# Performance work log

Measured on AMD Instinct MI355X. Metric: run time of the kernel, lower is better.

The kernel has to match this reference:

```python
import jax, jax.numpy as jnp
import numpy as np

TWOPI = 2.0 * np.pi


def setup_inputs() -> dict:
    key = jax.random.key(0)
    B, N, C = 16, 2048, 256
    x = jax.random.normal(key, (B, N, C), dtype=jnp.float32)
    return {"x": x}


def reference(x) -> jnp.ndarray:
    # Real-cosine DFT along dim 1: out[b,k,c] = sum_n x[b,n,c] * cos(-2*pi*n*k/N)
    # Equivalent to the original broadcast+sum but expressed as a GEMM with the
    # precomputed (N, N) cosine matrix (avoids the B*N*N*C intermediate).
    N = x.shape[1]
    n = jnp.arange(N, dtype=x.dtype)
    term = -TWOPI * n[None, :] * n[:, None] / N  # (k, n)
    cos_mat = jnp.cos(term)
    return jnp.einsum('kn,bnc->bkc', cos_mat, x)
```

## Files before the change

### kernel.cpp

```cpp
#include <hip/hip_runtime.h>
#include <hip/hip_bf16.h>
#include <math.h>

typedef __bf16 bf16_t;
typedef __attribute__((ext_vector_type(8))) __bf16 bf16x8;
typedef __attribute__((ext_vector_type(4))) float f32x4;

#define NN 2048
#define CC 256
#define BB 16
#define COLS 4096

#define KEE 320
#define MEE 256
#define KEO 256
#define KO  512

#define ANG2 (6.283185307179586f / 2048.0f)
#define ANG1 (6.283185307179586f / 1024.0f)
#define ANG0 (6.283185307179586f / 512.0f)

__device__ __forceinline__ void gload_lds16(const void* g, void* l) {
    __builtin_amdgcn_global_load_lds(
        (const __attribute__((address_space(1))) void*)g,
        (__attribute__((address_space(3))) void*)l, 16, 0, 0);
}

union V8 { bf16_t h[8]; uint4 v; };

#define NBLK_AEE 40
#define NBLK_AEO 32
#define NBLK_AO  128
#define NBLK_A   (NBLK_AEE + NBLK_AEO + NBLK_AO)
#define NBLK_FOLD 512
#define PREP_BLOCKS (NBLK_A + NBLK_FOLD + 64)

__global__ __launch_bounds__(256) void prep_kernel(
    const float* __restrict__ x,
    bf16_t* __restrict__ Aee, bf16_t* __restrict__ Aeo, bf16_t* __restrict__ Ao,
    bf16_t* __restrict__ Yee, bf16_t* __restrict__ Yeo, bf16_t* __restrict__ Yo)
{
    const int blk = blockIdx.x;
    const int t = threadIdx.x;

    if (blk < NBLK_AEE) {
        const int u = blk * 256 + t;
        const int i = u / 40;
        const int p0 = (u - i * 40) * 8;
        const unsigned step = (unsigned)i & 511u;
        unsigned ph = ((unsigned)i * (unsigned)p0) & 511u;
        V8 vals;
#pragma unroll
        for (int q = 0; q < 8; ++q) {
            vals.h[q] = (p0 + q <= 256) ? (bf16_t)cosf((float)ph * ANG0) : (bf16_t)0.0f;
            ph = (ph + step) & 511u;
        }
        *reinterpret_cast<uint4*>(Aee + (size_t)i * KEE + p0) = vals.v;
        return;
    }
    if (blk < NBLK_AEE + NBLK_AEO) {
        const int u = (blk - NBLK_AEE) * 256 + t;
        const int i = u >> 5;
        const int m0 = (u & 31) * 8;
        const unsigned tw = 2u * (unsigned)i + 1u;
        unsigned ph = ((unsigned)m0 * tw) & 1023u;
        V8 vals;
#pragma unroll
        for (int q = 0; q < 8; ++q) {
            vals.h[q] = (bf16_t)cosf((float)ph * ANG1);
            ph = (ph + tw) & 1023u;
        }
        *reinterpret_cast<uint4*>(Aeo + (size_t)i * KEO + m0) = vals.v;
        return;
    }
    if (blk < NBLK_A) {
        const int u = (blk - NBLK_AEE - NBLK_AEO) * 256 + t;
        const int j = u >> 6;
        const int u0 = (u & 63) * 8;
        const unsigned tw = 2u * (unsigned)j + 1u;
        V8 vals;
#pragma unroll
        for (int q = 0; q < 8; ++q) {
            const int uu = u0 + q;
            const int m = (uu <= 256) ? uu : (768 - uu);
            const unsigned ph = ((unsigned)m * tw) & 2047u;
            vals.h[q] = (bf16_t)cosf((float)ph * ANG2);
        }
        *reinterpret_cast<uint4*>(Ao + (size_t)j * KO + u0) = vals.v;
        return;
    }

    if (blk < NBLK_A + NBLK_FOLD) {
        const int f = blk - NBLK_A;
        const int pt = f >> 6;
        const int ct = f & 63;
        const int gc0 = ct * 64;
        const int col = t & 63;
        const int pg = t >> 6;
        const int p_base = pt * 32 + pg * 8;
        const float* xcol = x + (size_t)(gc0 >> 8) * NN * CC + (gc0 & 255) + col;

        float eeV[8], eoV[8], olV[8], ohV[8];
#pragma unroll
        for (int q = 0; q < 8; ++q) {
            const int p = p_base + q;
            const int n2 = 512 - p, n3 = 512 + p, n4 = 1024 - p;
            const int n5 = 1024 + p, n6 = 1536 - p, n7 = 1536 + p;
            const int n8 = (2048 - p) & 2047;
            const float x1 = xcol[(size_t)p  * CC];
            const float x2 = xcol[(size_t)n2 * CC];
            const float x3 = xcol[(size_t)n3 * CC];
            const float x4 = xcol[(size_t)n4 * CC];
            const float x5 = xcol[(size_t)n5 * CC];
            const float x6 = xcol[(size_t)n6 * CC];
            const float x7 = xcol[(size_t)n7 * CC];
            const float x8 = xcol[(size_t)n8 * CC];
            const float w = (p == 0) ? 0.5f : 1.0f;
            const float e_lo = w * ((x1 + x4) + (x5 + x8));
            const float e_hi = w * ((x2 + x3) + (x6 + x7));
            olV[q] = w * ((x1 - x5) - (x4 - x8));
            ohV[q] = (x2 - x6) - (x3 - x7);
            eeV[q] = e_lo + e_hi;
            eoV[q] = e_lo - e_hi;
        }
        if (pt == 0 && pg == 0) {
            const float a = xcol[(size_t)256  * CC];
            const float b2 = xcol[(size_t)768  * CC];
            const float c = xcol[(size_t)1280 * CC];
            const float d = xcol[(size_t)1792 * CC];
            ohV[0] = (a - c) - (b2 - d);
        }
        V8 vee, veo, vol, voh;
#pragma unroll
        for (int q = 0; q < 8; ++q) {
            vee.h[q] = (bf16_t)eeV[q]; veo.h[q] = (bf16_t)eoV[q];
            vol.h[q] = (bf16_t)olV[q]; voh.h[q] = (bf16_t)ohV[q];
        }
        const size_t gcol = (size_t)(gc0 + col);
        *reinterpret_cast<uint4*>(Yee + gcol * KEE + p_base) = vee.v;
        *reinterpret_cast<uint4*>(Yeo + gcol * KEO + p_base) = veo.v;
        *reinterpret_cast<uint4*>(Yo  + gcol * KO  + p_base) = vol.v;
        *reinterpret_cast<uint4*>(Yo  + gcol * KO  + 256 + p_base) = voh.v;
        return;
    }

    {
        const int ct = blk - (NBLK_A + NBLK_FOLD);
        if (t >= 64) return;
        const int gc0 = ct * 64;
        const float* xcol = x + (size_t)(gc0 >> 8) * NN * CC + (gc0 & 255) + t;
        const float ee256 = (xcol[(size_t)256 * CC] + xcol[(size_t)768 * CC]) +
                            (xcol[(size_t)1280 * CC] + xcol[(size_t)1792 * CC]);
        bf16_t* base = Yee + (size_t)(gc0 + t) * KEE + 256;
        V8 z; z.v = make_uint4(0, 0, 0, 0);
        V8 first = z; first.h[0] = (bf16_t)ee256;
        *reinterpret_cast<uint4*>(base) = first.v;
#pragma unroll
        for (int ch = 1; ch < 8; ++ch)
            *reinterpret_cast<uint4*>(base + ch * 8) = z.v;
    }
}


__global__ __launch_bounds__(256) void gemm_kernel(
    const bf16_t* __restrict__ Aee, const bf16_t* __restrict__ Aeo,
    const bf16_t* __restrict__ Ao,
    const bf16_t* __restrict__ Yee, const bf16_t* __restrict__ Yeo,
    const bf16_t* __restrict__ Yo, float* __restrict__ out)
{
    __shared__ bf16_t As[128 * 64];
    __shared__ bf16_t Bs[64 * 64];
    __shared__ float red[64][4];

    const int col0 = blockIdx.x * 64;
    const int yb = blockIdx.y;
    const int t = threadIdx.x;

    if (yb == 12) {
        const int col = t & 63;
        const int part = t >> 6;
        const bf16_t* yc = Yee + (size_t)(col0 + col) * KEE + part * 80;
        float s = 0.f;
#pragma unroll
        for (int jc = 0; jc < 10; ++jc) {
            const bf16x8 v = *reinterpret_cast<const bf16x8*>(yc + jc * 8);
#pragma unroll
            for (int q = 0; q < 8; ++q)
                s += (q & 1) ? -(float)v[q] : (float)v[q];
        }
        red[col][part] = s;
        __syncthreads();
        if (t < 64) {
            const float tot = (red[t][0] + red[t][1]) + (red[t][2] + red[t][3]);
            const int gc = col0 + t;
            out[(size_t)(gc >> 8) * NN * CC + (size_t)1024 * CC + (gc & 255)] = tot;
        }
        return;
    }

    const bf16_t *Ab, *Bb;
    int row0, kdim, half;
    if (yb < 4)      { half = 0; row0 = yb * 64;        kdim = KEE; Ab = Aee + (size_t)row0 * KEE; Bb = Yee + (size_t)col0 * KEE; }
    else if (yb < 8) { half = 1; row0 = (yb - 4) * 64;  kdim = KEO; Ab = Aeo + (size_t)row0 * KEO; Bb = Yeo + (size_t)col0 * KEO; }
    else             { half = 2; row0 = (yb - 8) * 128; kdim = KO;  Ab = Ao  + (size_t)row0 * KO;  Bb = Yo  + (size_t)col0 * KO; }
    const int ksteps = kdim >> 6;

    const int lane = t & 63;
    const int wid = t >> 6;
    const int wr = wid >> 1, wc = wid & 1;
    const int srow = t >> 3;
    const int scol = (t & 7) * 8;
    const int lrow = lane & 15;
    const int rgrp = lane >> 4;
    const int cl = lane & 15;

    if (half == 2) {
        f32x4 acc[4][2] = {};
        for (int kt = 0; kt < 8; ++kt) {
            const int k0 = kt * 64;
            __syncthreads();
#pragma unroll
            for (int it = 0; it < 4; ++it) {
                const int r = srow + it * 32;
                gload_lds16(Ab + (size_t)r * KO + k0 + scol, As + r * 64 + scol);
            }
#pragma unroll
            for (int it = 0; it < 2; ++it) {
                const int r = srow + it * 32;
                gload_lds16(Bb + (size_t)r * KO + k0 + scol, Bs + r * 64 + scol);
            }
            __syncthreads();
#pragma unroll
            for (int kk = 0; kk < 64; kk += 32) {
                const int koff = kk + (lane >> 4) * 8;
                bf16x8 af[4], bfr[2];
#pragma unroll
                for (int m = 0; m < 4; ++m)
                    af[m] = *(const bf16x8*)&As[(wr * 64 + m * 16 + lrow) * 64 + koff];
#pragma unroll
                for (int n = 0; n < 2; ++n)
                    bfr[n] = *(const bf16x8*)&Bs[(wc * 32 + n * 16 + lrow) * 64 + koff];
#pragma unroll
                for (int m = 0; m < 4; ++m)
#pragma unroll
                    for (int n = 0; n < 2; ++n)
                        acc[m][n] = __builtin_amdgcn_mfma_f32_16x16x32_bf16(
                            af[m], bfr[n], acc[m][n], 0, 0, 0);
            }
        }
#pragma unroll
        for (int m = 0; m < 4; ++m)
#pragma unroll
            for (int n = 0; n < 2; ++n) {
                const int col = col0 + wc * 32 + n * 16 + cl;
                float* obc = out + (size_t)(col >> 8) * NN * CC + (col & 255);
#pragma unroll
                for (int r = 0; r < 4; ++r) {
                    const int j = row0 + wr * 64 + m * 16 + rgrp * 4 + r;
                    const float v = acc[m][n][r];
                    obc[(size_t)(2 * j + 1) * CC] = v;
                    obc[(size_t)(2047 - 2 * j) * CC] = v;
                }
            }
    } else {
        f32x4 acc[2][2] = {};
        for (int kt = 0; kt < ksteps; ++kt) {
            const int k0 = kt * 64;
            __syncthreads();
#pragma unroll
            for (int it = 0; it < 2; ++it) {
                const int r = srow + it * 32;
                gload_lds16(Ab + (size_t)r * kdim + k0 + scol, As + r * 64 + scol);
                gload_lds16(Bb + (size_t)r * kdim + k0 + scol, Bs + r * 64 + scol);
            }
            __syncthreads();
#pragma unroll
            for (int kk = 0; kk < 64; kk += 32) {
                const int koff = kk + (lane >> 4) * 8;
                bf16x8 af[2], bfr[2];
#pragma unroll
                for (int m = 0; m < 2; ++m)
                    af[m] = *(const bf16x8*)&As[(wr * 32 + m * 16 + lrow) * 64 + koff];
#pragma unroll
                for (int n = 0; n < 2; ++n)
                    bfr[n] = *(const bf16x8*)&Bs[(wc * 32 + n * 16 + lrow) * 64 + koff];
#pragma unroll
                for (int m = 0; m < 2; ++m)
#pragma unroll
                    for (int n = 0; n < 2; ++n)
                        acc[m][n] = __builtin_amdgcn_mfma_f32_16x16x32_bf16(
                            af[m], bfr[n], acc[m][n], 0, 0, 0);
            }
        }
#pragma unroll
        for (int m = 0; m < 2; ++m)
#pragma unroll
            for (int n = 0; n < 2; ++n) {
                const int col = col0 + wc * 32 + n * 16 + cl;
                float* obc = out + (size_t)(col >> 8) * NN * CC + (col & 255);
#pragma unroll
                for (int r = 0; r < 4; ++r) {
                    const int i = row0 + wr * 32 + m * 16 + rgrp * 4 + r;
                    const float v = acc[m][n][r];
                    if (half == 0) {
                        obc[(size_t)(4 * i) * CC] = v;
                        if (i >= 1) obc[(size_t)(2048 - 4 * i) * CC] = v;
                    } else {
                        obc[(size_t)(4 * i + 2) * CC] = v;
                        obc[(size_t)(2046 - 4 * i) * CC] = v;
                    }
                }
            }
    }
}


__global__ void fallback_kernel(const float* __restrict__ x, float* __restrict__ out) {
    __shared__ float tbl[NN];
    const int b = blockIdx.y;
    const int kbase = blockIdx.x * 16;
    const int t = threadIdx.x;
    for (int i = t; i < NN; i += 256)
        tbl[i] = cosf((float)i * ANG2);
    __syncthreads();
    float acc[16];
#pragma unroll
    for (int kk = 0; kk < 16; ++kk) acc[kk] = 0.f;
    const float* xb = x + (size_t)b * NN * CC;
    for (int n = 0; n < NN; ++n) {
        const float xv = xb[(size_t)n * CC + t];
#pragma unroll
        for (int kk = 0; kk < 16; ++kk) {
            const int m = (n * (kbase + kk)) & (NN - 1);
            acc[kk] += tbl[m] * xv;
        }
    }
#pragma unroll
    for (int kk = 0; kk < 16; ++kk)
        out[((size_t)b * NN + kbase + kk) * CC + t] = acc[kk];
}

extern "C" void kernel_launch(void* const* d_in, const int* in_sizes, int n_in,
                              void* d_out, int out_size, void* d_ws, size_t ws_size,
                              hipStream_t stream) {
    const float* x = (const float*)d_in[0];
    float* out = (float*)d_out;

    const size_t Aee_b = (size_t)MEE * KEE * 2;
    const size_t Aeo_b = (size_t)256 * KEO * 2;
    const size_t Ao_b  = (size_t)512 * KO  * 2;
    const size_t Yee_b = (size_t)COLS * KEE * 2;
    const size_t Yeo_b = (size_t)COLS * KEO * 2;
    const size_t Yo_b  = (size_t)COLS * KO  * 2;
    const size_t need = Aee_b + Aeo_b + Ao_b + Yee_b + Yeo_b + Yo_b;

    if (ws_size >= need) {
        char* p = (char*)d_ws;
        bf16_t* Aee = (bf16_t*)p;              p += Aee_b;
        bf16_t* Aeo = (bf16_t*)p;              p += Aeo_b;
        bf16_t* Ao  = (bf16_t*)p;              p += Ao_b;
        bf16_t* Yee = (bf16_t*)p;              p += Yee_b;
        bf16_t* Yeo = (bf16_t*)p;              p += Yeo_b;
        bf16_t* Yo  = (bf16_t*)p;
        prep_kernel<<<PREP_BLOCKS, 256, 0, stream>>>(x, Aee, Aeo, Ao, Yee, Yeo, Yo);
        gemm_kernel<<<dim3(COLS / 64, 13), 256, 0, stream>>>(Aee, Aeo, Ao, Yee, Yeo, Yo, out);
    } else {
        fallback_kernel<<<dim3(NN / 16, BB), CC, 0, stream>>>(x, out);
    }
}
```

Before: 28.19 us.

## Double-buffer LDS tiles and XOR-swizzle K chunks to avoid bank conflicts

The GEMM main loops now use two LDS buffers: the next K tile is prefetched with global_load_lds while MFMAs run on the current tile, leaving one barrier per step instead of two. The global source column is XOR-permuted by row so that each LDS row holds its 8-element chunks in swizzled order. Fragment reads apply the matching XOR, which is meant to reduce LDS bank conflicts. LDS use doubles to roughly 48KB per block, which may lower occupancy.

```diff
diff --git a/kernel.cpp b/kernel.cpp
--- a/kernel.cpp
+++ b/kernel.cpp
@@ -168,8 +168,8 @@
     const bf16_t* __restrict__ Yee, const bf16_t* __restrict__ Yeo,
     const bf16_t* __restrict__ Yo, float* __restrict__ out)
 {
-    __shared__ bf16_t As[128 * 64];
-    __shared__ bf16_t Bs[64 * 64];
+    __shared__ bf16_t As[2][128 * 64];
+    __shared__ bf16_t Bs[2][64 * 64];
     __shared__ float red[64][4];
 
     const int col0 = blockIdx.x * 64;
@@ -209,37 +209,52 @@
     const int wid = t >> 6;
     const int wr = wid >> 1, wc = wid & 1;
     const int srow = t >> 3;
-    const int scol = (t & 7) * 8;
+    const int sc_chunk = t & 7;
+    const int s_swz = (sc_chunk ^ (srow & 7)) * 8;
+    const int lds_lin = srow * 64 + sc_chunk * 8;
     const int lrow = lane & 15;
+    const int rx8 = lrow & 7;
     const int rgrp = lane >> 4;
     const int cl = lane & 15;
+    const int hi8 = (lane >> 4) * 8;
 
     if (half == 2) {
         f32x4 acc[4][2] = {};
+        int cur = 0;
+#pragma unroll
+        for (int it = 0; it < 4; ++it)
+            gload_lds16(Ab + (size_t)(srow + it * 32) * KO + s_swz,
+                        &As[0][lds_lin + it * 2048]);
+#pragma unroll
+        for (int it = 0; it < 2; ++it)
+            gload_lds16(Bb + (size_t)(srow + it * 32) * KO + s_swz,
+                        &Bs[0][lds_lin + it * 2048]);
+        __syncthreads();
         for (int kt = 0; kt < 8; ++kt) {
-            const int k0 = kt * 64;
-            __syncthreads();
-#pragma unroll
-            for (int it = 0; it < 4; ++it) {
-                const int r = srow + it * 32;
-                gload_lds16(Ab + (size_t)r * KO + k0 + scol, As + r * 64 + scol);
-            }
-#pragma unroll
-            for (int it = 0; it < 2; ++it) {
-                const int r = srow + it * 32;
-                gload_lds16(Bb + (size_t)r * KO + k0 + scol, Bs + r * 64 + scol);
-            }
-            __syncthreads();
+            if (kt + 1 < 8) {
+                const int k0 = (kt + 1) * 64;
+#pragma unroll
+                for (int it = 0; it < 4; ++it)
+                    gload_lds16(Ab + (size_t)(srow + it * 32) * KO + k0 + s_swz,
+                                &As[cur ^ 1][lds_lin + it * 2048]);
+#pragma unroll
+                for (int it = 0; it < 2; ++it)
+                    gload_lds16(Bb + (size_t)(srow + it * 32) * KO + k0 + s_swz,
+                                &Bs[cur ^ 1][lds_lin + it * 2048]);
+            }
+            const bf16_t* as = &As[cur][0];
+            const bf16_t* bs = &Bs[cur][0];
 #pragma unroll
             for (int kk = 0; kk < 64; kk += 32) {
-                const int koff = kk + (lane >> 4) * 8;
+                const int g = (kk + hi8) >> 3;
+                const int rc = ((g ^ rx8) * 8);
                 bf16x8 af[4], bfr[2];
 #pragma unroll
                 for (int m = 0; m < 4; ++m)
-                    af[m] = *(const bf16x8*)&As[(wr * 64 + m * 16 + lrow) * 64 + koff];
+                    af[m] = *(const bf16x8*)&as[(wr * 64 + m * 16 + lrow) * 64 + rc];
 #pragma unroll
                 for (int n = 0; n < 2; ++n)
-                    bfr[n] = *(const bf16x8*)&Bs[(wc * 32 + n * 16 + lrow) * 64 + koff];
+                    bfr[n] = *(const bf16x8*)&bs[(wc * 32 + n * 16 + lrow) * 64 + rc];
 #pragma unroll
                 for (int m = 0; m < 4; ++m)
 #pragma unroll
@@ -247,6 +262,8 @@
                         acc[m][n] = __builtin_amdgcn_mfma_f32_16x16x32_bf16(
                             af[m], bfr[n], acc[m][n], 0, 0, 0);
             }
+            __syncthreads();
+            cur ^= 1;
         }
 #pragma unroll
         for (int m = 0; m < 4; ++m)
@@ -264,26 +281,37 @@
             }
     } else {
         f32x4 acc[2][2] = {};
+        int cur = 0;
+#pragma unroll
+        for (int it = 0; it < 2; ++it) {
+            const size_t ro = (size_t)(srow + it * 32) * kdim + s_swz;
+            gload_lds16(Ab + ro, &As[0][lds_lin + it * 2048]);
+            gload_lds16(Bb + ro, &Bs[0][lds_lin + it * 2048]);
+        }
+        __syncthreads();
         for (int kt = 0; kt < ksteps; ++kt) {
-            const int k0 = kt * 64;
-            __syncthreads();
-#pragma unroll
-            for (int it = 0; it < 2; ++it) {
-                const int r = srow + it * 32;
-                gload_lds16(Ab + (size_t)r * kdim + k0 + scol, As + r * 64 + scol);
-                gload_lds16(Bb + (size_t)r * kdim + k0 + scol, Bs + r * 64 + scol);
-            }
-            __syncthreads();
+            if (kt + 1 < ksteps) {
+                const int k0 = (kt + 1) * 64;
+#pragma unroll
+                for (int it = 0; it < 2; ++it) {
+                    const size_t ro = (size_t)(srow + it * 32) * kdim + k0 + s_swz;
+                    gload_lds16(Ab + ro, &As[cur ^ 1][lds_lin + it * 2048]);
+                    gload_lds16(Bb + ro, &Bs[cur ^ 1][lds_lin + it * 2048]);
+                }
+            }
+            const bf16_t* as = &As[cur][0];
+            const bf16_t* bs = &Bs[cur][0];
 #pragma unroll
             for (int kk = 0; kk < 64; kk += 32) {
-                const int koff = kk + (lane >> 4) * 8;
+                const int g = (kk + hi8) >> 3;
+                const int rc = ((g ^ rx8) * 8);
                 bf16x8 af[2], bfr[2];
 #pragma unroll
                 for (int m = 0; m < 2; ++m)
-                    af[m] = *(const bf16x8*)&As[(wr * 32 + m * 16 + lrow) * 64 + koff];
+                    af[m] = *(const bf16x8*)&as[(wr * 32 + m * 16 + lrow) * 64 + rc];
 #pragma unroll
                 for (int n = 0; n < 2; ++n)
-                    bfr[n] = *(const bf16x8*)&Bs[(wc * 32 + n * 16 + lrow) * 64 + koff];
+                    bfr[n] = *(const bf16x8*)&bs[(wc * 32 + n * 16 + lrow) * 64 + rc];
 #pragma unroll
                 for (int m = 0; m < 2; ++m)
 #pragma unroll
@@ -291,6 +319,8 @@
                         acc[m][n] = __builtin_amdgcn_mfma_f32_16x16x32_bf16(
                             af[m], bfr[n], acc[m][n], 0, 0, 0);
             }
+            __syncthreads();
+            cur ^= 1;
         }
 #pragma unroll
         for (int m = 0; m < 2; ++m)
```

Result: faster. 26.90 us, median of 2 (-4.6%).

## Fuse input fold and GEMM into one kernel with per-column-tile spin barrier

Applied to the files above, without the earlier changes.

Splits cosine-table construction into its own small kernel and merges the input fold with the GEMM into one 256-block, 512-thread kernel. Blocks sharing a column tile sync through a global atomic counter, then each computes a 256x64 output slab using double-buffered, XOR-swizzled LDS tiles fed by global_load_lds. This is meant to remove a kernel boundary and to overlap loads with MFMA compute. In exchange it adds a memset launch, a spin-wait that relies on all 256 blocks being co-resident, and uneven work across blocks.

```diff
diff --git a/kernel.cpp b/kernel.cpp
--- a/kernel.cpp
+++ b/kernel.cpp
@@ -12,7 +12,6 @@
 #define COLS 4096
 
 #define KEE 320
-#define MEE 256
 #define KEO 256
 #define KO  512
 
@@ -32,13 +31,9 @@
 #define NBLK_AEO 32
 #define NBLK_AO  128
 #define NBLK_A   (NBLK_AEE + NBLK_AEO + NBLK_AO)
-#define NBLK_FOLD 512
-#define PREP_BLOCKS (NBLK_A + NBLK_FOLD + 64)
-
-__global__ __launch_bounds__(256) void prep_kernel(
-    const float* __restrict__ x,
-    bf16_t* __restrict__ Aee, bf16_t* __restrict__ Aeo, bf16_t* __restrict__ Ao,
-    bf16_t* __restrict__ Yee, bf16_t* __restrict__ Yeo, bf16_t* __restrict__ Yo)
+
+__global__ __launch_bounds__(256) void build_A_kernel(
+    bf16_t* __restrict__ Aee, bf16_t* __restrict__ Aeo, bf16_t* __restrict__ Ao)
 {
     const int blk = blockIdx.x;
     const int t = threadIdx.x;
@@ -73,7 +68,7 @@
         *reinterpret_cast<uint4*>(Aeo + (size_t)i * KEO + m0) = vals.v;
         return;
     }
-    if (blk < NBLK_A) {
+    {
         const int u = (blk - NBLK_AEE - NBLK_AEO) * 256 + t;
         const int j = u >> 6;
         const int u0 = (u & 63) * 8;
@@ -87,23 +82,123 @@
             vals.h[q] = (bf16_t)cosf((float)ph * ANG2);
         }
         *reinterpret_cast<uint4*>(Ao + (size_t)j * KO + u0) = vals.v;
-        return;
-    }
-
-    if (blk < NBLK_A + NBLK_FOLD) {
-        const int f = blk - NBLK_A;
-        const int pt = f >> 6;
-        const int ct = f & 63;
+    }
+}
+
+__device__ __forceinline__ void section512(
+    const bf16_t* __restrict__ Ab, const bf16_t* __restrict__ Bb,
+    const int K, const int ksteps, const int mode, const int row0,
+    const int col0, float* __restrict__ out,
+    bf16_t (&As)[2][16384], bf16_t (&Bs)[2][4096], const int t)
+{
+    const int lane = t & 63;
+    const int w = t >> 6;
+    const int wr = w >> 1, wc = w & 1;
+    const int srow = t >> 3;
+    const int schunk = t & 7;
+    const int s_swz = (schunk ^ (srow & 7)) * 8;
+    const int lds_lin = srow * 64 + schunk * 8;
+    const int lrow = lane & 15;
+    const int rx8 = lrow & 7;
+    const int rgrp = lane >> 4;
+    const int hi8 = rgrp * 8;
+    const int cl = lane & 15;
+
+    f32x4 acc[4][2] = {};
+    int cur = 0;
+#pragma unroll
+    for (int it = 0; it < 4; ++it)
+        gload_lds16(Ab + (size_t)(srow + it * 64) * K + s_swz,
+                    &As[0][lds_lin + it * 4096]);
+    gload_lds16(Bb + (size_t)srow * K + s_swz, &Bs[0][lds_lin]);
+    __syncthreads();
+    for (int kt = 0; kt < ksteps; ++kt) {
+        if (kt + 1 < ksteps) {
+            const int k0 = (kt + 1) * 64;
+#pragma unroll
+            for (int it = 0; it < 4; ++it)
+                gload_lds16(Ab + (size_t)(srow + it * 64) * K + k0 + s_swz,
+                            &As[cur ^ 1][lds_lin + it * 4096]);
+            gload_lds16(Bb + (size_t)srow * K + k0 + s_swz, &Bs[cur ^ 1][lds_lin]);
+        }
+        const bf16_t* as = &As[cur][0];
+        const bf16_t* bs = &Bs[cur][0];
+#pragma unroll
+        for (int kk = 0; kk < 64; kk += 32) {
+            const int g = (kk + hi8) >> 3;
+            const int rc = (g ^ rx8) * 8;
+            bf16x8 af[4], bfr[2];
+#pragma unroll
+            for (int m = 0; m < 4; ++m)
+                af[m] = *(const bf16x8*)&as[(wr * 64 + m * 16 + lrow) * 64 + rc];
+#pragma unroll
+            for (int n = 0; n < 2; ++n)
+                bfr[n] = *(const bf16x8*)&bs[(wc * 32 + n * 16 + lrow) * 64 + rc];
+#pragma unroll
+            for (int m = 0; m < 4; ++m)
+#pragma unroll
+                for (int n = 0; n < 2; ++n)
+                    acc[m][n] = __builtin_amdgcn_mfma_f32_16x16x32_bf16(
+                        af[m], bfr[n], acc[m][n], 0, 0, 0);
+        }
+        __syncthreads();
+        cur ^= 1;
+    }
+#pragma unroll
+    for (int m = 0; m < 4; ++m)
+#pragma unroll
+        for (int n = 0; n < 2; ++n) {
+            const int col = col0 + wc * 32 + n * 16 + cl;
+            float* obc = out + (size_t)(col >> 8) * NN * CC + (col & 255);
+#pragma unroll
+            for (int r = 0; r < 4; ++r) {
+                const int i = wr * 64 + m * 16 + rgrp * 4 + r;
+                const float v = acc[m][n][r];
+                if (mode == 0) {
+                    obc[(size_t)(4 * i) * CC] = v;
+                    if (i >= 1) obc[(size_t)(2048 - 4 * i) * CC] = v;
+                } else if (mode == 1) {
+                    obc[(size_t)(4 * i + 2) * CC] = v;
+                    obc[(size_t)(2046 - 4 * i) * CC] = v;
+                } else {
+                    const int j = row0 + i;
+                    obc[(size_t)(2 * j + 1) * CC] = v;
+                    obc[(size_t)(2047 - 2 * j) * CC] = v;
+                }
+            }
+        }
+}
+
+__global__ __launch_bounds__(512) void mono_kernel(
+    const float* __restrict__ x,
+    const bf16_t* __restrict__ Aee, const bf16_t* __restrict__ Aeo,
+    const bf16_t* __restrict__ Ao,
+    bf16_t* __restrict__ Yee, bf16_t* __restrict__ Yeo, bf16_t* __restrict__ Yo,
+    float* __restrict__ out, unsigned* __restrict__ ctcnt)
+{
+    __shared__ bf16_t As[2][16384];
+    __shared__ bf16_t Bs[2][4096];
+    __shared__ float red[64][8];
+
+    const int bid = blockIdx.x;
+    const int ct = bid & 63;
+    const int q  = bid >> 6;
+    const int t  = threadIdx.x;
+    const int th = t & 255;
+    const int halfq = t >> 8;
+
+    {
+        const int pt = 2 * q + halfq;
         const int gc0 = ct * 64;
-        const int col = t & 63;
-        const int pg = t >> 6;
+        const int col = th & 63;
+        const int pg = th >> 6;
         const int p_base = pt * 32 + pg * 8;
         const float* xcol = x + (size_t)(gc0 >> 8) * NN * CC + (gc0 & 255) + col;
 
         float eeV[8], eoV[8], olV[8], ohV[8];
 #pragma unroll
-        for (int q = 0; q < 8; ++q) {
-            const int p = p_base + q;
+        for (int qq = 0; qq < 8; ++qq) {
+            const int p = p_base + qq;
             const int n2 = 512 - p, n3 = 512 + p, n4 = 1024 - p;
             const int n5 = 1024 + p, n6 = 1536 - p, n7 = 1536 + p;
             const int n8 = (2048 - p) & 2047;
@@ -118,39 +213,35 @@
             const float w = (p == 0) ? 0.5f : 1.0f;
             const float e_lo = w * ((x1 + x4) + (x5 + x8));
             const float e_hi = w * ((x2 + x3) + (x6 + x7));
-            olV[q] = w * ((x1 - x5) - (x4 - x8));
-            ohV[q] = (x2 - x6) - (x3 - x7);
-            eeV[q] = e_lo + e_hi;
-            eoV[q] = e_lo - e_hi;
+            olV[qq] = w * ((x1 - x5) - (x4 - x8));
+            ohV[qq] = (x2 - x6) - (x3 - x7);
+            eeV[qq] = e_lo + e_hi;
+            eoV[qq] = e_lo - e_hi;
         }
         if (pt == 0 && pg == 0) {
-            const float a = xcol[(size_t)256  * CC];
+            const float a  = xcol[(size_t)256  * CC];
             const float b2 = xcol[(size_t)768  * CC];
-            const float c = xcol[(size_t)1280 * CC];
-            const float d = xcol[(size_t)1792 * CC];
+            const float c  = xcol[(size_t)1280 * CC];
+            const float d  = xcol[(size_t)1792 * CC];
             ohV[0] = (a - c) - (b2 - d);
         }
         V8 vee, veo, vol, voh;
 #pragma unroll
-        for (int q = 0; q < 8; ++q) {
-            vee.h[q] = (bf16_t)eeV[q]; veo.h[q] = (bf16_t)eoV[q];
-            vol.h[q] = (bf16_t)olV[q]; voh.h[q] = (bf16_t)ohV[q];
+        for (int qq = 0; qq < 8; ++qq) {
+            vee.h[qq] = (bf16_t)eeV[qq]; veo.h[qq] = (bf16_t)eoV[qq];
+            vol.h[qq] = (bf16_t)olV[qq]; voh.h[qq] = (bf16_t)ohV[qq];
         }
         const size_t gcol = (size_t)(gc0 + col);
         *reinterpret_cast<uint4*>(Yee + gcol * KEE + p_base) = vee.v;
         *reinterpret_cast<uint4*>(Yeo + gcol * KEO + p_base) = veo.v;
         *reinterpret_cast<uint4*>(Yo  + gcol * KO  + p_base) = vol.v;
         *reinterpret_cast<uint4*>(Yo  + gcol * KO  + 256 + p_base) = voh.v;
-        return;
-    }
-
-    {
-        const int ct = blk - (NBLK_A + NBLK_FOLD);
-        if (t >= 64) return;
+    }
+    if (q == 0 && t < 64) {
         const int gc0 = ct * 64;
-        const float* xcol = x + (size_t)(gc0 >> 8) * NN * CC + (gc0 & 255) + t;
-        const float ee256 = (xcol[(size_t)256 * CC] + xcol[(size_t)768 * CC]) +
-                            (xcol[(size_t)1280 * CC] + xcol[(size_t)1792 * CC]);
+        const float* xc2 = x + (size_t)(gc0 >> 8) * NN * CC + (gc0 & 255) + t;
+        const float ee256 = (xc2[(size_t)256 * CC] + xc2[(size_t)768 * CC]) +
+                            (xc2[(size_t)1280 * CC] + xc2[(size_t)1792 * CC]);
         bf16_t* base = Yee + (size_t)(gc0 + t) * KEE + 256;
         V8 z; z.v = make_uint4(0, 0, 0, 0);
         V8 first = z; first.h[0] = (bf16_t)ee256;
@@ -159,158 +250,45 @@
         for (int ch = 1; ch < 8; ++ch)
             *reinterpret_cast<uint4*>(base + ch * 8) = z.v;
     }
-}
-
-
-__global__ __launch_bounds__(256) void gemm_kernel(
-    const bf16_t* __restrict__ Aee, const bf16_t* __restrict__ Aeo,
-    const bf16_t* __restrict__ Ao,
-    const bf16_t* __restrict__ Yee, const bf16_t* __restrict__ Yeo,
-    const bf16_t* __restrict__ Yo, float* __restrict__ out)
-{
-    __shared__ bf16_t As[128 * 64];
-    __shared__ bf16_t Bs[64 * 64];
-    __shared__ float red[64][4];
-
-    const int col0 = blockIdx.x * 64;
-    const int yb = blockIdx.y;
-    const int t = threadIdx.x;
-
-    if (yb == 12) {
-        const int col = t & 63;
-        const int part = t >> 6;
-        const bf16_t* yc = Yee + (size_t)(col0 + col) * KEE + part * 80;
-        float s = 0.f;
-#pragma unroll
-        for (int jc = 0; jc < 10; ++jc) {
-            const bf16x8 v = *reinterpret_cast<const bf16x8*>(yc + jc * 8);
-#pragma unroll
-            for (int q = 0; q < 8; ++q)
-                s += (q & 1) ? -(float)v[q] : (float)v[q];
-        }
-        red[col][part] = s;
-        __syncthreads();
-        if (t < 64) {
-            const float tot = (red[t][0] + red[t][1]) + (red[t][2] + red[t][3]);
-            const int gc = col0 + t;
-            out[(size_t)(gc >> 8) * NN * CC + (size_t)1024 * CC + (gc & 255)] = tot;
-        }
-        return;
-    }
-
-    const bf16_t *Ab, *Bb;
-    int row0, kdim, half;
-    if (yb < 4)      { half = 0; row0 = yb * 64;        kdim = KEE; Ab = Aee + (size_t)row0 * KEE; Bb = Yee + (size_t)col0 * KEE; }
-    else if (yb < 8) { half = 1; row0 = (yb - 4) * 64;  kdim = KEO; Ab = Aeo + (size_t)row0 * KEO; Bb = Yeo + (size_t)col0 * KEO; }
-    else             { half = 2; row0 = (yb - 8) * 128; kdim = KO;  Ab = Ao  + (size_t)row0 * KO;  Bb = Yo  + (size_t)col0 * KO; }
-    const int ksteps = kdim >> 6;
-
-    const int lane = t & 63;
-    const int wid = t >> 6;
-    const int wr = wid >> 1, wc = wid & 1;
-    const int srow = t >> 3;
-    const int scol = (t & 7) * 8;
-    const int lrow = lane & 15;
-    const int rgrp = lane >> 4;
-    const int cl = lane & 15;
-
-    if (half == 2) {
-        f32x4 acc[4][2] = {};
-        for (int kt = 0; kt < 8; ++kt) {
-            const int k0 = kt * 64;
+
+    __syncthreads();
+    if (t == 0) {
+        __threadfence();
+        atomicAdd(&ctcnt[ct], 1u);
+        while (atomicAdd(&ctcnt[ct], 0u) < 4u) __builtin_amdgcn_s_sleep(2);
+        __threadfence();
+    }
+    __syncthreads();
+
+    const int col0 = ct * 64;
+    if (q < 2) {
+        section512(Ao + (size_t)q * 256 * KO, Yo + (size_t)col0 * KO,
+                   KO, 8, 2, q * 256, col0, out, As, Bs, t);
+    } else if (q == 2) {
+        section512(Aee, Yee + (size_t)col0 * KEE, KEE, 5, 0, 0, col0, out, As, Bs, t);
+        {
+            const int col = t & 63, part = t >> 6;
+            const bf16_t* yc = Yee + (size_t)(col0 + col) * KEE + part * 40;
+            float s = 0.f;
+#pragma unroll
+            for (int jc = 0; jc < 5; ++jc) {
+                const bf16x8 v = *reinterpret_cast<const bf16x8*>(yc + jc * 8);
+#pragma unroll
+                for (int qq = 0; qq < 8; ++qq)
+                    s += (qq & 1) ? -(float)v[qq] : (float)v[qq];
+            }
+            red[col][part] = s;
             __syncthreads();
-#pragma unroll
-            for (int it = 0; it < 4; ++it) {
-                const int r = srow + it * 32;
-                gload_lds16(Ab + (size_t)r * KO + k0 + scol, As + r * 64 + scol);
+            if (t < 64) {
+                float tot = 0.f;
+#pragma unroll
+                for (int p2 = 0; p2 < 8; ++p2) tot += red[t][p2];
+                const int gc = col0 + t;
+                out[(size_t)(gc >> 8) * NN * CC + (size_t)1024 * CC + (gc & 255)] = tot;
             }
-#pragma unroll
-            for (int it = 0; it < 2; ++it) {
-                const int r = srow + it * 32;
-                gload_lds16(Bb + (size_t)r * KO + k0 + scol, Bs + r * 64 + scol);
-            }
-            __syncthreads();
-#pragma unroll
-            for (int kk = 0; kk < 64; kk += 32) {
-                const int koff = kk + (lane >> 4) * 8;
-                bf16x8 af[4], bfr[2];
-#pragma unroll
-                for (int m = 0; m < 4; ++m)
-                    af[m] = *(const bf16x8*)&As[(wr * 64 + m * 16 + lrow) * 64 + koff];
-#pragma unroll
-                for (int n = 0; n < 2; ++n)
-                    bfr[n] = *(const bf16x8*)&Bs[(wc * 32 + n * 16 + lrow) * 64 + koff];
-#pragma unroll
-                for (int m = 0; m < 4; ++m)
-#pragma unroll
-                    for (int n = 0; n < 2; ++n)
-                        acc[m][n] = __builtin_amdgcn_mfma_f32_16x16x32_bf16(
-                            af[m], bfr[n], acc[m][n], 0, 0, 0);
-            }
-        }
-#pragma unroll
-        for (int m = 0; m < 4; ++m)
-#pragma unroll
-            for (int n = 0; n < 2; ++n) {
-                const int col = col0 + wc * 32 + n * 16 + cl;
-                float* obc = out + (size_t)(col >> 8) * NN * CC + (col & 255);
-#pragma unroll
-                for (int r = 0; r < 4; ++r) {
-                    const int j = row0 + wr * 64 + m * 16 + rgrp * 4 + r;
-                    const float v = acc[m][n][r];
-                    obc[(size_t)(2 * j + 1) * CC] = v;
-                    obc[(size_t)(2047 - 2 * j) * CC] = v;
-                }
-            }
+        }
     } else {
-        f32x4 acc[2][2] = {};
-        for (int kt = 0; kt < ksteps; ++kt) {
-            const int k0 = kt * 64;
-            __syncthreads();
-#pragma unroll
-            for (int it = 0; it < 2; ++it) {
-                const int r = srow + it * 32;
-                gload_lds16(Ab + (size_t)r * kdim + k0 + scol, As + r * 64 + scol);
-                gload_lds16(Bb + (size_t)r * kdim + k0 + scol, Bs + r * 64 + scol);
-            }
-            __syncthreads();
-#pragma unroll
-            for (int kk = 0; kk < 64; kk += 32) {
-                const int koff = kk + (lane >> 4) * 8;
-                bf16x8 af[2], bfr[2];
-#pragma unroll
-                for (int m = 0; m < 2; ++m)
-                    af[m] = *(const bf16x8*)&As[(wr * 32 + m * 16 + lrow) * 64 + koff];
-#pragma unroll
-                for (int n = 0; n < 2; ++n)
-                    bfr[n] = *(const bf16x8*)&Bs[(wc * 32 + n * 16 + lrow) * 64 + koff];
-#pragma unroll
-                for (int m = 0; m < 2; ++m)
-#pragma unroll
-                    for (int n = 0; n < 2; ++n)
-                        acc[m][n] = __builtin_amdgcn_mfma_f32_16x16x32_bf16(
-                            af[m], bfr[n], acc[m][n], 0, 0, 0);
-            }
-        }
-#pragma unroll
-        for (int m = 0; m < 2; ++m)
-#pragma unroll
-            for (int n = 0; n < 2; ++n) {
-                const int col = col0 + wc * 32 + n * 16 + cl;
-                float* obc = out + (size_t)(col >> 8) * NN * CC + (col & 255);
-#pragma unroll
-                for (int r = 0; r < 4; ++r) {
-                    const int i = row0 + wr * 32 + m * 16 + rgrp * 4 + r;
-                    const float v = acc[m][n][r];
-                    if (half == 0) {
-                        obc[(size_t)(4 * i) * CC] = v;
-                        if (i >= 1) obc[(size_t)(2048 - 4 * i) * CC] = v;
-                    } else {
-                        obc[(size_t)(4 * i + 2) * CC] = v;
-                        obc[(size_t)(2046 - 4 * i) * CC] = v;
-                    }
-                }
-            }
+        section512(Aeo, Yeo + (size_t)col0 * KEO, KEO, 4, 1, 0, col0, out, As, Bs, t);
     }
 }
 
@@ -346,13 +324,14 @@
     const float* x = (const float*)d_in[0];
     float* out = (float*)d_out;
 
-    const size_t Aee_b = (size_t)MEE * KEE * 2;
+    const size_t Aee_b = (size_t)256 * KEE * 2;
     const size_t Aeo_b = (size_t)256 * KEO * 2;
     const size_t Ao_b  = (size_t)512 * KO  * 2;
     const size_t Yee_b = (size_t)COLS * KEE * 2;
     const size_t Yeo_b = (size_t)COLS * KEO * 2;
     const size_t Yo_b  = (size_t)COLS * KO  * 2;
-    const size_t need = Aee_b + Aeo_b + Ao_b + Yee_b + Yeo_b + Yo_b;
+    const size_t cnt_b = 64 * sizeof(unsigned);
+    const size_t need = Aee_b + Aeo_b + Ao_b + Yee_b + Yeo_b + Yo_b + cnt_b;
 
     if (ws_size >= need) {
         char* p = (char*)d_ws;
@@ -361,9 +340,11 @@
         bf16_t* Ao  = (bf16_t*)p;              p += Ao_b;
         bf16_t* Yee = (bf16_t*)p;              p += Yee_b;
         bf16_t* Yeo = (bf16_t*)p;              p += Yeo_b;
-        bf16_t* Yo  = (bf16_t*)p;
-        prep_kernel<<<PREP_BLOCKS, 256, 0, stream>>>(x, Aee, Aeo, Ao, Yee, Yeo, Yo);
-        gemm_kernel<<<dim3(COLS / 64, 13), 256, 0, stream>>>(Aee, Aeo, Ao, Yee, Yeo, Yo, out);
+        bf16_t* Yo  = (bf16_t*)p;              p += Yo_b;
+        unsigned* ctcnt = (unsigned*)p;
+        hipMemsetAsync(ctcnt, 0, cnt_b, stream);
+        build_A_kernel<<<NBLK_A, 256, 0, stream>>>(Aee, Aeo, Ao);
+        mono_kernel<<<256, 512, 0, stream>>>(x, Aee, Aeo, Ao, Yee, Yeo, Yo, out, ctcnt);
     } else {
         fallback_kernel<<<dim3(NN / 16, BB), CC, 0, stream>>>(x, out);
     }
```

Result: slower. 55.32 us (+96.3%).
